# Performance work log

Measured on AMD Instinct MI355X. Metric: run time of the kernel, lower is better.

Reference implementation:

```python
import jax, jax.numpy as jnp
import numpy as np

B, T, EMB = 2, 2048, 2048
NH, NKV, HD, VHD = 16, 4, 128, 128
N_REP = NH // NKV
ROPE_DIM, ROPE_THETA = 64, 10000.0
WIN = 1024
MLPD = 8192
CS = 2048  # cache size == T: single prefill fills the cache
K_MASK = jnp.finfo(jnp.bfloat16).min
SCALING = HD ** -0.5


def _rope_sincos(positions, rope_dim, theta):
    fraction = jnp.arange(0, rope_dim, 2, dtype=jnp.float32) / rope_dim
    inv_freq = 1.0 / (theta ** fraction)
    ang = jnp.einsum('BT,k->BTk', positions.astype(jnp.float32), inv_freq,
                     precision=jax.lax.Precision.HIGHEST)
    sin, cos = jnp.sin(ang), jnp.cos(ang)
    return jnp.concatenate([sin, sin], -1), jnp.concatenate([cos, cos], -1)


def _rotate_half(x):
    h = x.shape[-1] // 2
    return jnp.concatenate([-x[..., h:], x[..., :h]], -1)


def _apply_rope_partial(x, sin, cos, rope_dim):
    x_rope, x_nope = x[..., :rope_dim], x[..., rope_dim:]
    s, c = sin[:, :, None, :], cos[:, :, None, :]
    x_rope = x_rope * c + _rotate_half(x_rope) * s
    return jnp.concatenate([x_rope, x_nope], -1).astype(x.dtype)


def _rms_norm(x, scale, eps=1e-6):
    xf = x.astype(jnp.float32)
    var = jnp.mean(jnp.square(xf), axis=-1, keepdims=True)
    return (xf * jax.lax.rsqrt(var + eps) * (1.0 + scale)).astype(x.dtype)


def _repeat_kv(h, n_rep):
    if n_rep == 1:
        return h
    b, s, k, d = h.shape
    return jnp.repeat(h[:, :, :, None, :], n_rep, axis=3).reshape(b, s, k * n_rep, d)


def setup_inputs() -> dict:
    key = jax.random.key(0)
    ks = jax.random.split(key, 12)
    s = 0.02
    return {
        'x': jax.random.normal(ks[0], (B, T, EMB), jnp.float32),
        'segment_ids': jnp.ones((B, T), jnp.int32),
        'wq': jax.random.normal(ks[1], (EMB, NH, HD), jnp.float32) * s,
        'wk': jax.random.normal(ks[2], (EMB, NKV, HD), jnp.float32) * s,
        'wv': jax.random.normal(ks[3], (EMB, NKV, VHD), jnp.float32) * s,
        'wo': jax.random.normal(ks[4], (NH, VHD, EMB), jnp.float32) * s,
        'sink_bias': jax.random.normal(ks[5], (NH,), jnp.float32) * s,
        'gate_w': jax.random.normal(ks[6], (EMB, MLPD), jnp.float32) * s,
        'up_w': jax.random.normal(ks[7], (EMB, MLPD), jnp.float32) * s,
        'down_w': jax.random.normal(ks[8], (MLPD, EMB), jnp.float32) * s,
        'norm1_scale': jax.random.normal(ks[9], (EMB,), jnp.float32) * s,
        'norm2_scale': jax.random.normal(ks[10], (EMB,), jnp.float32) * s,
        'k_cache': jnp.zeros((B, CS, NKV, HD), jnp.float32),
        'v_cache': jnp.zeros((B, CS, NKV, VHD), jnp.float32),
    }


def reference(x, segment_ids, wq, wk, wv, wo, sink_bias, gate_w, up_w, down_w,
              norm1_scale, norm2_scale, k_cache, v_cache):
    b, t, _ = x.shape
    cs = k_cache.shape[1]
    cur_ind = jnp.zeros((), jnp.int32)  # fresh cache (prefill)

    # --- attention branch (pre-norm) ---
    h = _rms_norm(x, norm1_scale)
    q = jnp.einsum('BTD,DNH->BTNH', h, wq)
    k = jnp.einsum('BSD,DKH->BSKH', h, wk)
    v = jnp.einsum('BSD,DKV->BSKV', h, wv)

    left_pads = jnp.sum(jnp.cumsum(segment_ids != 0, axis=-1) == 0, -1).astype(jnp.int32)
    start_ind = left_pads  # start_ind initialized to -1 -> set to left_pads
    ar = jnp.arange(t, dtype=jnp.int32)
    first = jnp.argmax(segment_ids, axis=1).astype(jnp.int32)
    positions = jnp.where(segment_ids != 0, ar[None, :] - first[:, None], 2 ** 30) + cur_ind

    sin, cos = _rope_sincos(positions, ROPE_DIM, ROPE_THETA)
    q = _apply_rope_partial(q, sin, cos, ROPE_DIM)
    k = _apply_rope_partial(k, sin, cos, ROPE_DIM)

    k_cache = jax.lax.dynamic_update_slice(k_cache, k, (0, cur_ind, 0, 0))
    v_cache = jax.lax.dynamic_update_slice(v_cache, v, (0, cur_ind, 0, 0))

    kc = _repeat_kv(k_cache, N_REP)  # [B,S,N,H]
    vc = _repeat_kv(v_cache, N_REP)  # [B,S,N,V]

    attn_logits = jnp.einsum('BTNH,BSNH->BTNS', q, kc) * SCALING

    q_pos = cur_ind + ar[None, :] - start_ind[:, None]                      # [B,T]
    ts = jnp.arange(cs, dtype=jnp.int32)
    kv_segment_ids = (ts[None, :] >= start_ind[:, None]) & (ts[None, :] < cur_ind + t)
    k_pos = ts[None, :] - start_ind[:, None]                                # [B,S]
    causal_mask = k_pos[:, None, :] <= q_pos[:, :, None]
    segment_mask = kv_segment_ids[:, None, :] == segment_ids[:, :, None]
    window_mask = k_pos[:, None, :] >= q_pos[:, :, None] - (WIN - 1)
    final_mask = causal_mask & segment_mask & window_mask                    # [B,T,S]

    attn_logits = jnp.where(final_mask[:, :, None, :], attn_logits, K_MASK)

    # learned sink bias: extra logit column, dropped after softmax
    sink = jnp.broadcast_to(sink_bias[None, None, :, None], (b, t, NH, 1))
    attn_logits = jnp.concatenate([attn_logits, sink], axis=-1)
    attn_weights = jax.nn.softmax(attn_logits.astype(jnp.float32), axis=-1).astype(attn_logits.dtype)
    attn_weights = attn_weights[..., :-1]

    attn_out = jnp.einsum('BTNS,BSNV->BTNV', attn_weights, vc)
    attn_out = jnp.einsum('BTNV,NVD->BTD', attn_out, wo)

    x = x + attn_out

    # --- MLP branch (pre-norm, SwiGLU) ---
    h = _rms_norm(x, norm2_scale)
    mlp_out = (jax.nn.silu(h @ gate_w) * (h @ up_w)) @ down_w
    return x + mlp_out
```

## Files before the change

### kernel.cpp

```cpp
#include <hip/hip_runtime.h>
#include <hip/hip_bf16.h>
#include <stdint.h>

#define B_    2
#define T_    2048
#define EMB_  2048
#define NH_   16
#define NKV_  4
#define HD_   128
#define MLPD_ 8192
#define WIN_  1024
#define BT_   (B_ * T_)
#define QKVN_ 3072

typedef __bf16 bf16;
typedef __bf16 bf16x8 __attribute__((ext_vector_type(8)));
typedef float  f32x4  __attribute__((ext_vector_type(4)));

__device__ __forceinline__ bf16 f2b(float f) {
  __hip_bfloat16 h = __float2bfloat16(f);
  return *reinterpret_cast<bf16*>(&h);
}
__device__ __forceinline__ float b2f(bf16 b) {
  __hip_bfloat16 h = *reinterpret_cast<__hip_bfloat16*>(&b);
  return __bfloat162float(h);
}

__device__ __forceinline__ void load_lds16(const void* g, void* l) {
  __builtin_amdgcn_global_load_lds(
      (const __attribute__((address_space(1))) void*)g,
      (__attribute__((address_space(3))) void*)l, 16, 0, 0);
}

__device__ __forceinline__ void swz(int& mt, int& nt) {
  const int gridN = gridDim.x;
  const int lin = blockIdx.y * gridN + blockIdx.x;
  const int per = 8 * gridN;
  const int grp = lin / per, rem = lin % per;
  mt = (grp << 3) + (rem & 7);
  nt = rem >> 3;
}

__global__ __launch_bounds__(256) void transpose_kernel(
    const float* __restrict__ in, bf16* __restrict__ out, int R, int C)
{
  __shared__ float tile[32][33];
  const int tx = threadIdx.x, ty = threadIdx.y;
  const int c0 = blockIdx.x * 32, r0 = blockIdx.y * 32;
  #pragma unroll
  for (int i = 0; i < 32; i += 8)
    tile[ty + i][tx] = in[(long)(r0 + ty + i) * C + c0 + tx];
  __syncthreads();
  #pragma unroll
  for (int i = 0; i < 32; i += 8)
    out[(long)(c0 + ty + i) * R + r0 + tx] = f2b(tile[tx][ty + i]);
}

__global__ __launch_bounds__(256) void rmsnorm_kernel(
    const float* __restrict__ x, const float* __restrict__ scale,
    bf16* __restrict__ out)
{
  const long row = blockIdx.x;
  const float* xr = x + row * EMB_;
  bf16* orow = out + row * EMB_;
  const float4 v0 = ((const float4*)xr)[threadIdx.x];
  const float4 v1 = ((const float4*)xr)[threadIdx.x + 256];
  float ss = v0.x*v0.x + v0.y*v0.y + v0.z*v0.z + v0.w*v0.w
           + v1.x*v1.x + v1.y*v1.y + v1.z*v1.z + v1.w*v1.w;
  #pragma unroll
  for (int off = 32; off >= 1; off >>= 1) ss += __shfl_xor(ss, off, 64);
  __shared__ float red[4];
  if ((threadIdx.x & 63) == 0) red[threadIdx.x >> 6] = ss;
  __syncthreads();
  const float tot = red[0] + red[1] + red[2] + red[3];
  const float rs = rsqrtf(tot * (1.0f / EMB_) + 1e-6f);
  const float4 s0 = ((const float4*)scale)[threadIdx.x];
  const float4 s1 = ((const float4*)scale)[threadIdx.x + 256];
  const int c0 = threadIdx.x * 4;
  orow[c0 + 0]    = f2b(v0.x * rs * (1.0f + s0.x));
  orow[c0 + 1]    = f2b(v0.y * rs * (1.0f + s0.y));
  orow[c0 + 2]    = f2b(v0.z * rs * (1.0f + s0.z));
  orow[c0 + 3]    = f2b(v0.w * rs * (1.0f + s0.w));
  orow[c0 + 1024] = f2b(v1.x * rs * (1.0f + s1.x));
  orow[c0 + 1025] = f2b(v1.y * rs * (1.0f + s1.y));
  orow[c0 + 1026] = f2b(v1.z * rs * (1.0f + s1.z));
  orow[c0 + 1027] = f2b(v1.w * rs * (1.0f + s1.w));
}

template <int EPI>
__global__ __launch_bounds__(256) void gemm_kernel(
    const bf16* __restrict__ A, const bf16* __restrict__ Bt,
    void* __restrict__ out, const float* __restrict__ res,
    int M, int N, int K)
{
  __shared__ __align__(16) bf16 As[128 * 32];
  __shared__ __align__(16) bf16 Bs[128 * 32];
  const int tid  = threadIdx.x;
  const int wave = tid >> 6, lane = tid & 63;
  int mt, nt; swz(mt, nt);
  const int bm = mt << 7, bn = nt << 7;
  const int wm = (wave & 1) << 6, wn = (wave >> 1) << 6;
  const int l16 = lane & 15, quad = lane >> 4;
  const int srow = lane >> 2, scol = (lane & 3) << 3;

  const bf16* Ap = A  + (long)(bm + wave * 32 + srow) * K + scol;
  const bf16* Bp = Bt + (long)(bn + wave * 32 + srow) * K + scol;
  char* ldsA = (char*)As + wave * 2048;
  char* ldsB = (char*)Bs + wave * 2048;

  f32x4 acc[4][4] = {};

  for (int k0 = 0; k0 < K; k0 += 32) {
    __syncthreads();
    #pragma unroll
    for (int j = 0; j < 2; ++j) {
      load_lds16(Ap + (long)j * 16 * K + k0, ldsA + j * 1024);
      load_lds16(Bp + (long)j * 16 * K + k0, ldsB + j * 1024);
    }
    __syncthreads();
    bf16x8 af[4], bfr[4];
    #pragma unroll
    for (int i = 0; i < 4; ++i) {
      af[i]  = *(const bf16x8*)&As[(wm + i * 16 + l16) * 32 + quad * 8];
      bfr[i] = *(const bf16x8*)&Bs[(wn + i * 16 + l16) * 32 + quad * 8];
    }
    #pragma unroll
    for (int mb = 0; mb < 4; ++mb)
      #pragma unroll
      for (int nb = 0; nb < 4; ++nb)
        acc[mb][nb] = __builtin_amdgcn_mfma_f32_16x16x32_bf16(af[mb], bfr[nb], acc[mb][nb], 0, 0, 0);
  }

  const int crow = bm + wm + (quad << 2);
  const int ccol = bn + wn + l16;
  #pragma unroll
  for (int mb = 0; mb < 4; ++mb)
    #pragma unroll
    for (int nb = 0; nb < 4; ++nb)
      #pragma unroll
      for (int r = 0; r < 4; ++r) {
        const long idx = (long)(crow + mb * 16 + r) * N + (ccol + nb * 16);
        const float v = acc[mb][nb][r];
        if (EPI == 0) {
          ((bf16*)out)[idx] = f2b(v);
        } else {
          ((float*)out)[idx] = v + res[idx];
        }
      }
}

__global__ __launch_bounds__(512) void mlp_gateup_kernel(
    const bf16* __restrict__ A, const bf16* __restrict__ Bg,
    const bf16* __restrict__ Bu, bf16* __restrict__ out,
    int M, int N, int K)
{
  __shared__ __align__(16) char smem[32768];
  const int tid = threadIdx.x;
  const int wave = tid >> 6, lane = tid & 63;
  const int role = wave >> 2, wq = wave & 3;
  const int wm = (wq & 1) << 6, wn = (wq >> 1) << 6;
  const int l16 = lane & 15, quad = lane >> 4;
  const int srow = lane >> 2, scol = (lane & 3) << 3;

  int mt, nt; swz(mt, nt);
  const int bm = mt << 7, bn = nt << 7;

  const bf16* sp[3]; char* dp[3];
  #pragma unroll
  for (int j = 0; j < 3; ++j) {
    const int c = 3 * wave + j;
    const int buf = c >> 3, r0 = (c & 7) << 4;
    const bf16* gbase = (buf == 0) ? A + (long)bm * K
                      : (buf == 1) ? Bg + (long)bn * K
                                   : Bu + (long)bn * K;
    sp[j] = gbase + (long)(r0 + srow) * K + scol;
    dp[j] = smem + buf * 8192 + (c & 7) * 1024;
  }
  const bf16* Asb = (const bf16*)smem;
  const bf16* Bsb = (const bf16*)(smem + 8192 + role * 8192);

  f32x4 acc[4][4] = {};

  for (int k0 = 0; k0 < K; k0 += 32) {
    __syncthreads();
    #pragma unroll
    for (int j = 0; j < 3; ++j) load_lds16(sp[j] + k0, dp[j]);
    __syncthreads();
    bf16x8 af[4], bfr[4];
    #pragma unroll
    for (int i = 0; i < 4; ++i) {
      af[i]  = *(const bf16x8*)&Asb[(wm + i * 16 + l16) * 32 + quad * 8];
      bfr[i] = *(const bf16x8*)&Bsb[(wn + i * 16 + l16) * 32 + quad * 8];
    }
    #pragma unroll
    for (int mb = 0; mb < 4; ++mb)
      #pragma unroll
      for (int nb = 0; nb < 4; ++nb)
        acc[mb][nb] = __builtin_amdgcn_mfma_f32_16x16x32_bf16(af[mb], bfr[nb], acc[mb][nb], 0, 0, 0);
  }

  __syncthreads();
  bf16* Ex = (bf16*)smem;
  const int rw = wm + (quad << 2), cw = wn + l16;
  if (role == 0) {
    #pragma unroll
    for (int mb = 0; mb < 4; ++mb)
      #pragma unroll
      for (int nb = 0; nb < 4; ++nb)
        #pragma unroll
        for (int r = 0; r < 4; ++r) {
          const float g = acc[mb][nb][r];
          Ex[(rw + mb * 16 + r) * 128 + cw + nb * 16] = f2b(g / (1.0f + __expf(-g)));
        }
  }
  __syncthreads();
  if (role == 1) {
    #pragma unroll
    for (int mb = 0; mb < 4; ++mb)
      #pragma unroll
      for (int nb = 0; nb < 4; ++nb)
        #pragma unroll
        for (int r = 0; r < 4; ++r) {
          const float sg = b2f(Ex[(rw + mb * 16 + r) * 128 + cw + nb * 16]);
          out[(long)(bm + rw + mb * 16 + r) * N + bn + cw + nb * 16] =
              f2b(acc[mb][nb][r] * sg);
        }
  }
}

__global__ __launch_bounds__(256) void rope_kernel(
    const bf16* __restrict__ qkv, bf16* __restrict__ Q,
    bf16* __restrict__ K, bf16* __restrict__ VT)
{
  const int t = blockIdx.x, b = blockIdx.y;
  const bf16* row = qkv + (long)(b * T_ + t) * QKVN_;
  const float tf = (float)t;
  for (int idx = threadIdx.x; idx < NH_ * HD_; idx += 256) {
    const int head = idx >> 7, hd = idx & 127;
    const float v = b2f(row[idx]);
    float o;
    if (hd < 64) {
      const int j = hd & 31;
      const float ang = tf * expf(-(float)j * 0.28782313662425574f);
      const float sn = sinf(ang), cs = cosf(ang);
      o = (hd < 32) ? (v * cs - b2f(row[idx + 32]) * sn)
                    : (v * cs + b2f(row[idx - 32]) * sn);
    } else o = v;
    Q[((long)(b * NH_ + head) * T_ + t) * HD_ + hd] = f2b(o);
  }
  for (int idx = threadIdx.x; idx < NKV_ * HD_; idx += 256) {
    const int kv = idx >> 7, hd = idx & 127;
    const float v = b2f(row[NH_ * HD_ + idx]);
    float o;
    if (hd < 64) {
      const int j = hd & 31;
      const float ang = tf * expf(-(float)j * 0.28782313662425574f);
      const float sn = sinf(ang), cs = cosf(ang);
      o = (hd < 32) ? (v * cs - b2f(row[NH_ * HD_ + idx + 32]) * sn)
                    : (v * cs + b2f(row[NH_ * HD_ + idx - 32]) * sn);
    } else o = v;
    K[((long)(b * NKV_ + kv) * T_ + t) * HD_ + hd] = f2b(o);
  }
  for (int idx = threadIdx.x; idx < NKV_ * HD_; idx += 256) {
    const int kv = idx >> 7, vd = idx & 127;
    VT[((long)(b * NKV_ + kv) * HD_ + vd) * T_ + t] = row[(NH_ + NKV_) * HD_ + idx];
  }
}

__global__ __launch_bounds__(256) void attn_kernel(
    const bf16* __restrict__ Q, const bf16* __restrict__ Kg,
    const bf16* __restrict__ VTg, const float* __restrict__ sink,
    bf16* __restrict__ attnb)
{
  __shared__ __align__(16) bf16 Qs[64 * 136];
  __shared__ __align__(16) bf16 Ks[64 * 136];
  __shared__ __align__(16) bf16 Vs[128 * 72];
  __shared__ __align__(16) bf16 Ps[64 * 72];

  const int qt = blockIdx.x;
  const int bh = blockIdx.y;
  const int b = bh >> 4, h = bh & 15;
  const int kvh = h >> 2;
  const int t0 = qt * 64;
  const int tid = threadIdx.x;
  const int wave = tid >> 6, lane = tid & 63;
  const int quad = lane >> 4, l16 = lane & 15;

  const bf16* Qp = Q + ((long)(b * NH_ + h) * T_ + t0) * HD_;
  #pragma unroll
  for (int c = tid; c < 1024; c += 256) {
    const int r = c >> 4, cc = (c & 15) << 3;
    *(uint4*)&Qs[r * 136 + cc] = *(const uint4*)&Qp[r * HD_ + cc];
  }

  float m_i[4], l_i[4];
  const float sb = sink[h];
  #pragma unroll
  for (int r = 0; r < 4; ++r) { m_i[r] = sb; l_i[r] = 1.0f; }
  f32x4 Oacc[8] = {};

  const int st_lo = (qt > 16) ? (qt - 16) : 0;
  for (int st = st_lo; st <= qt; ++st) {
    const int s0 = st * 64;
    __syncthreads();
    const bf16* Kp = Kg + ((long)(b * NKV_ + kvh) * T_ + s0) * HD_;
    #pragma unroll
    for (int c = tid; c < 1024; c += 256) {
      const int r = c >> 4, cc = (c & 15) << 3;
      *(uint4*)&Ks[r * 136 + cc] = *(const uint4*)&Kp[r * HD_ + cc];
    }
    const bf16* Vp = VTg + (long)(b * NKV_ + kvh) * HD_ * T_ + s0;
    #pragma unroll
    for (int c = tid; c < 1024; c += 256) {
      const int r = c >> 3, cc = (c & 7) << 3;
      *(uint4*)&Vs[r * 72 + cc] = *(const uint4*)&Vp[(long)r * T_ + cc];
    }
    __syncthreads();

    f32x4 sacc[4] = {};
    #pragma unroll
    for (int kb = 0; kb < 4; ++kb) {
      const bf16x8 aq = *(const bf16x8*)&Qs[(wave * 16 + l16) * 136 + kb * 32 + quad * 8];
      #pragma unroll
      for (int nb = 0; nb < 4; ++nb) {
        const bf16x8 bk = *(const bf16x8*)&Ks[(nb * 16 + l16) * 136 + kb * 32 + quad * 8];
        sacc[nb] = __builtin_amdgcn_mfma_f32_16x16x32_bf16(aq, bk, sacc[nb], 0, 0, 0);
      }
    }

    float sv[4][4];
    float rmax[4] = {-INFINITY, -INFINITY, -INFINITY, -INFINITY};
    const int colb = s0 + l16;
    const int rowb = t0 + wave * 16 + quad * 4;
    #pragma unroll
    for (int nb = 0; nb < 4; ++nb)
      #pragma unroll
      for (int r = 0; r < 4; ++r) {
        float v = sacc[nb][r] * 0.08838834764831845f;
        const int s = colb + nb * 16, tq = rowb + r;
        if (s > tq || s < tq - (WIN_ - 1)) v = -INFINITY;
        sv[nb][r] = v;
        rmax[r] = fmaxf(rmax[r], v);
      }
    #pragma unroll
    for (int r = 0; r < 4; ++r)
      #pragma unroll
      for (int off = 1; off < 16; off <<= 1)
        rmax[r] = fmaxf(rmax[r], __shfl_xor(rmax[r], off, 64));
    float alpha[4], rsum[4];
    #pragma unroll
    for (int r = 0; r < 4; ++r) {
      const float mn = fmaxf(m_i[r], rmax[r]);
      alpha[r] = __expf(m_i[r] - mn);
      m_i[r] = mn;
      rsum[r] = 0.0f;
    }
    #pragma unroll
    for (int nb = 0; nb < 4; ++nb)
      #pragma unroll
      for (int r = 0; r < 4; ++r) {
        const float p = __expf(sv[nb][r] - m_i[r]);
        rsum[r] += p;
        Ps[(wave * 16 + quad * 4 + r) * 72 + nb * 16 + l16] = f2b(p);
      }
    #pragma unroll
    for (int r = 0; r < 4; ++r) {
      #pragma unroll
      for (int off = 1; off < 16; off <<= 1)
        rsum[r] += __shfl_xor(rsum[r], off, 64);
      l_i[r] = l_i[r] * alpha[r] + rsum[r];
    }
    #pragma unroll
    for (int nb = 0; nb < 8; ++nb)
      #pragma unroll
      for (int r = 0; r < 4; ++r)
        Oacc[nb][r] *= alpha[r];
    __syncthreads();

    #pragma unroll
    for (int ks = 0; ks < 2; ++ks) {
      const bf16x8 ap = *(const bf16x8*)&Ps[(wave * 16 + l16) * 72 + ks * 32 + quad * 8];
      #pragma unroll
      for (int nb = 0; nb < 8; ++nb) {
        const bf16x8 bv = *(const bf16x8*)&Vs[(nb * 16 + l16) * 72 + ks * 32 + quad * 8];
        Oacc[nb] = __builtin_amdgcn_mfma_f32_16x16x32_bf16(ap, bv, Oacc[nb], 0, 0, 0);
      }
    }
  }

  float rcp[4];
  #pragma unroll
  for (int r = 0; r < 4; ++r) rcp[r] = 1.0f / l_i[r];
  bf16* outp = attnb + ((long)(b * T_ + t0 + wave * 16 + quad * 4)) * EMB_ + h * HD_ + l16;
  #pragma unroll
  for (int nb = 0; nb < 8; ++nb)
    #pragma unroll
    for (int r = 0; r < 4; ++r)
      outp[(long)r * EMB_ + nb * 16] = f2b(Oacc[nb][r] * rcp[r]);
}

extern "C" void kernel_launch(void* const* d_in, const int* in_sizes, int n_in,
                              void* d_out, int out_size, void* d_ws, size_t ws_size,
                              hipStream_t stream)
{
  (void)in_sizes; (void)n_in; (void)out_size; (void)ws_size;
  const float* x    = (const float*)d_in[0];
  const float* wq   = (const float*)d_in[2];
  const float* wk   = (const float*)d_in[3];
  const float* wv   = (const float*)d_in[4];
  const float* wo   = (const float*)d_in[5];
  const float* sink = (const float*)d_in[6];
  const float* gw   = (const float*)d_in[7];
  const float* uw   = (const float*)d_in[8];
  const float* dw   = (const float*)d_in[9];
  const float* n1   = (const float*)d_in[10];
  const float* n2   = (const float*)d_in[11];

  char* base = (char*)d_ws;
  bf16*  hbuf  = (bf16*)base;
  char*  R1    = base + (size_t)16777216;
  char*  R2    = R1   + (size_t)67108864;
  bf16*  mact  = (bf16*)(R2 + (size_t)33554432);

  bf16* qkv   = (bf16*)R1;
  bf16* Qb    = (bf16*)(R1 + 25165824);
  bf16* Kb    = (bf16*)(R1 + 41943040);
  bf16* VTb   = (bf16*)(R1 + 46137344);
  bf16* attnb = (bf16*)R1;
  bf16* wqkvT = (bf16*)R2;
  bf16* woT   = (bf16*)(R2 + 12582912);
  bf16* gateT = (bf16*)R1;
  bf16* upT   = (bf16*)(R1 + 33554432);
  bf16* downT = (bf16*)R2;
  float* x1   = (float*)d_out;

  const dim3 tb(32, 8);
  transpose_kernel<<<dim3( 64,  64), tb, 0, stream>>>(wq, wqkvT,                      EMB_, EMB_);
  transpose_kernel<<<dim3( 16,  64), tb, 0, stream>>>(wk, wqkvT + (size_t)2048*EMB_,  EMB_, 512);
  transpose_kernel<<<dim3( 16,  64), tb, 0, stream>>>(wv, wqkvT + (size_t)2560*EMB_,  EMB_, 512);
  transpose_kernel<<<dim3( 64,  64), tb, 0, stream>>>(wo, woT,                        EMB_, EMB_);

  rmsnorm_kernel<<<BT_, 256, 0, stream>>>(x, n1, hbuf);
  gemm_kernel<0><<<dim3(QKVN_/128, BT_/128), 256, 0, stream>>>(hbuf, wqkvT, qkv, nullptr, BT_, QKVN_, EMB_);
  rope_kernel<<<dim3(T_, B_), 256, 0, stream>>>(qkv, Qb, Kb, VTb);
  attn_kernel<<<dim3(T_/64, B_*NH_), 256, 0, stream>>>(Qb, Kb, VTb, sink, attnb);
  gemm_kernel<1><<<dim3(EMB_/128, BT_/128), 256, 0, stream>>>(attnb, woT, x1, x, BT_, EMB_, EMB_);

  rmsnorm_kernel<<<BT_, 256, 0, stream>>>(x1, n2, hbuf);
  transpose_kernel<<<dim3(256,  64), tb, 0, stream>>>(gw, gateT, EMB_, MLPD_);
  transpose_kernel<<<dim3(256,  64), tb, 0, stream>>>(uw, upT,   EMB_, MLPD_);
  mlp_gateup_kernel<<<dim3(MLPD_/128, BT_/128), 512, 0, stream>>>(hbuf, gateT, upT, mact, BT_, MLPD_, EMB_);
  transpose_kernel<<<dim3( 64, 256), tb, 0, stream>>>(dw, downT, MLPD_, EMB_);
  gemm_kernel<1><<<dim3(EMB_/128, BT_/128), 256, 0, stream>>>(mact, downT, (float*)d_out, x1, BT_, EMB_, MLPD_);
}
```

Measured before the change: 1.114 ms.

## Remove grid swizzle, deepen gate/up K-step, add 256-row down-projection kernel

Removes the grouped tile-order swizzle from the GEMM kernels so tiles map directly from the block indices. The gate/up kernel now loads a K-slab of 64 per iteration instead of 32, which halves the number of barrier pairs at the cost of 48KB of LDS. The down projection moves to a new 512-thread kernel that computes a 256x128 tile, so two wave groups share one B tile, cutting B traffic and block count. Dropping the swizzle may reduce L2 locality for the larger grids, and the extra LDS may lower occupancy.

```diff
diff --git a/kernel.cpp b/kernel.cpp
--- a/kernel.cpp
+++ b/kernel.cpp
@@ -30,15 +30,6 @@
   __builtin_amdgcn_global_load_lds(
       (const __attribute__((address_space(1))) void*)g,
       (__attribute__((address_space(3))) void*)l, 16, 0, 0);
-}
-
-__device__ __forceinline__ void swz(int& mt, int& nt) {
-  const int gridN = gridDim.x;
-  const int lin = blockIdx.y * gridN + blockIdx.x;
-  const int per = 8 * gridN;
-  const int grp = lin / per, rem = lin % per;
-  mt = (grp << 3) + (rem & 7);
-  nt = rem >> 3;
 }
 
 __global__ __launch_bounds__(256) void transpose_kernel(
@@ -97,8 +88,7 @@
   __shared__ __align__(16) bf16 Bs[128 * 32];
   const int tid  = threadIdx.x;
   const int wave = tid >> 6, lane = tid & 63;
-  int mt, nt; swz(mt, nt);
-  const int bm = mt << 7, bn = nt << 7;
+  const int bm = blockIdx.y << 7, bn = blockIdx.x << 7;
   const int wm = (wave & 1) << 6, wn = (wave >> 1) << 6;
   const int l16 = lane & 15, quad = lane >> 4;
   const int srow = lane >> 2, scol = (lane & 3) << 3;
@@ -154,7 +144,7 @@
     const bf16* __restrict__ Bu, bf16* __restrict__ out,
     int M, int N, int K)
 {
-  __shared__ __align__(16) char smem[32768];
+  __shared__ __align__(16) char smem[49152];
   const int tid = threadIdx.x;
   const int wave = tid >> 6, lane = tid & 63;
   const int role = wave >> 2, wq = wave & 3;
@@ -162,41 +152,43 @@
   const int l16 = lane & 15, quad = lane >> 4;
   const int srow = lane >> 2, scol = (lane & 3) << 3;
 
-  int mt, nt; swz(mt, nt);
-  const int bm = mt << 7, bn = nt << 7;
-
-  const bf16* sp[3]; char* dp[3];
-  #pragma unroll
-  for (int j = 0; j < 3; ++j) {
-    const int c = 3 * wave + j;
-    const int buf = c >> 3, r0 = (c & 7) << 4;
+  const int bm = blockIdx.y << 7, bn = blockIdx.x << 7;
+
+  const bf16* sp[6]; char* dp[6];
+  #pragma unroll
+  for (int j = 0; j < 6; ++j) {
+    const int c = 6 * wave + j;
+    const int buf = c >> 4, idx = c & 15, kh = idx >> 3, r8 = idx & 7;
     const bf16* gbase = (buf == 0) ? A + (long)bm * K
                       : (buf == 1) ? Bg + (long)bn * K
                                    : Bu + (long)bn * K;
-    sp[j] = gbase + (long)(r0 + srow) * K + scol;
-    dp[j] = smem + buf * 8192 + (c & 7) * 1024;
+    sp[j] = gbase + (long)(r8 * 16 + srow) * K + kh * 32 + scol;
+    dp[j] = smem + buf * 16384 + kh * 8192 + r8 * 1024;
   }
   const bf16* Asb = (const bf16*)smem;
-  const bf16* Bsb = (const bf16*)(smem + 8192 + role * 8192);
+  const bf16* Bsb = (const bf16*)(smem + 16384 + role * 16384);
 
   f32x4 acc[4][4] = {};
 
-  for (int k0 = 0; k0 < K; k0 += 32) {
-    __syncthreads();
-    #pragma unroll
-    for (int j = 0; j < 3; ++j) load_lds16(sp[j] + k0, dp[j]);
-    __syncthreads();
-    bf16x8 af[4], bfr[4];
-    #pragma unroll
-    for (int i = 0; i < 4; ++i) {
-      af[i]  = *(const bf16x8*)&Asb[(wm + i * 16 + l16) * 32 + quad * 8];
-      bfr[i] = *(const bf16x8*)&Bsb[(wn + i * 16 + l16) * 32 + quad * 8];
-    }
-    #pragma unroll
-    for (int mb = 0; mb < 4; ++mb)
-      #pragma unroll
-      for (int nb = 0; nb < 4; ++nb)
-        acc[mb][nb] = __builtin_amdgcn_mfma_f32_16x16x32_bf16(af[mb], bfr[nb], acc[mb][nb], 0, 0, 0);
+  for (int k0 = 0; k0 < K; k0 += 64) {
+    __syncthreads();
+    #pragma unroll
+    for (int j = 0; j < 6; ++j) load_lds16(sp[j] + k0, dp[j]);
+    __syncthreads();
+    #pragma unroll
+    for (int kh = 0; kh < 2; ++kh) {
+      bf16x8 af[4], bfr[4];
+      #pragma unroll
+      for (int i = 0; i < 4; ++i) {
+        af[i]  = *(const bf16x8*)&Asb[kh * 4096 + (wm + i * 16 + l16) * 32 + quad * 8];
+        bfr[i] = *(const bf16x8*)&Bsb[kh * 4096 + (wn + i * 16 + l16) * 32 + quad * 8];
+      }
+      #pragma unroll
+      for (int mb = 0; mb < 4; ++mb)
+        #pragma unroll
+        for (int nb = 0; nb < 4; ++nb)
+          acc[mb][nb] = __builtin_amdgcn_mfma_f32_16x16x32_bf16(af[mb], bfr[nb], acc[mb][nb], 0, 0, 0);
+    }
   }
 
   __syncthreads();
@@ -226,6 +218,68 @@
               f2b(acc[mb][nb][r] * sg);
         }
   }
+}
+
+__global__ __launch_bounds__(512) void down_kernel(
+    const bf16* __restrict__ A, const bf16* __restrict__ Bt,
+    float* __restrict__ out, const float* __restrict__ res,
+    int M, int N, int K)
+{
+  __shared__ __align__(16) char smem[24576];
+  const int tid = threadIdx.x;
+  const int wave = tid >> 6, lane = tid & 63;
+  const int role = wave >> 2, wq = wave & 3;
+  const int wm = (wq & 1) << 6, wn = (wq >> 1) << 6;
+  const int l16 = lane & 15, quad = lane >> 4;
+  const int srow = lane >> 2, scol = (lane & 3) << 3;
+
+  const int bm = blockIdx.y << 8, bn = blockIdx.x << 7;
+
+  const bf16* sp[3]; char* dp[3];
+  #pragma unroll
+  for (int j = 0; j < 3; ++j) {
+    const int c = 3 * wave + j;
+    const int buf = c >> 3, r0 = (c & 7) << 4;
+    const bf16* gbase = (buf == 0) ? A + (long)bm * K
+                      : (buf == 1) ? A + (long)(bm + 128) * K
+                                   : Bt + (long)bn * K;
+    sp[j] = gbase + (long)(r0 + srow) * K + scol;
+    dp[j] = smem + buf * 8192 + (c & 7) * 1024;
+  }
+  const bf16* Asb = (const bf16*)(smem + role * 8192);
+  const bf16* Bsb = (const bf16*)(smem + 16384);
+
+  f32x4 acc[4][4] = {};
+
+  for (int k0 = 0; k0 < K; k0 += 32) {
+    __syncthreads();
+    #pragma unroll
+    for (int j = 0; j < 3; ++j) load_lds16(sp[j] + k0, dp[j]);
+    __syncthreads();
+    bf16x8 af[4], bfr[4];
+    #pragma unroll
+    for (int i = 0; i < 4; ++i) {
+      af[i]  = *(const bf16x8*)&Asb[(wm + i * 16 + l16) * 32 + quad * 8];
+      bfr[i] = *(const bf16x8*)&Bsb[(wn + i * 16 + l16) * 32 + quad * 8];
+    }
+    #pragma unroll
+    for (int mb = 0; mb < 4; ++mb)
+      #pragma unroll
+      for (int nb = 0; nb < 4; ++nb)
+        acc[mb][nb] = __builtin_amdgcn_mfma_f32_16x16x32_bf16(af[mb], bfr[nb], acc[mb][nb], 0, 0, 0);
+  }
+
+  const int crow = bm + role * 128 + wm + (quad << 2);
+  const int ccol = bn + wn + l16;
+  #pragma unroll
+  for (int mb = 0; mb < 4; ++mb)
+    #pragma unroll
+    for (int nb = 0; nb < 4; ++nb)
+      #pragma unroll
+      for (int r = 0; r < 4; ++r) {
+        const long idx = (long)(crow + mb * 16 + r) * N + (ccol + nb * 16);
+        out[idx] = acc[mb][nb][r] + res[idx];
+      }
 }
 
 __global__ __launch_bounds__(256) void rope_kernel(
@@ -451,5 +505,5 @@
   transpose_kernel<<<dim3(256,  64), tb, 0, stream>>>(uw, upT,   EMB_, MLPD_);
   mlp_gateup_kernel<<<dim3(MLPD_/128, BT_/128), 512, 0, stream>>>(hbuf, gateT, upT, mact, BT_, MLPD_, EMB_);
   transpose_kernel<<<dim3( 64, 256), tb, 0, stream>>>(dw, downT, MLPD_, EMB_);
-  gemm_kernel<1><<<dim3(EMB_/128, BT_/128), 256, 0, stream>>>(mact, downT, (float*)d_out, x1, BT_, EMB_, MLPD_);
-}
+  down_kernel<<<dim3(EMB_/128, BT_/256), 512, 0, stream>>>(mact, downT, (float*)d_out, x1, BT_, EMB_, MLPD_);
+}
```

After: 1.104 ms. Within noise of the previous version (-0.9%).
